# Kernel optimization log

Measured on AMD Instinct MI355X. Metric: run time of the kernel, lower is better.

Reference implementation:

```python
import jax, jax.numpy as jnp
import numpy as np

B, T, C = 4, 2048, 1024
H = 16
HD = C // H  # 64


def setup_inputs() -> dict:
    key = jax.random.key(0)
    ks = jax.random.split(key, 5)
    s = 0.02
    return {
        "x": jax.random.normal(ks[0], (B, T, C), jnp.float32),
        "qkv_w": jax.random.normal(ks[1], (3 * C, C), jnp.float32) * s,
        "qkv_b": jax.random.normal(ks[2], (3 * C,), jnp.float32) * s,
        "out_w": jax.random.normal(ks[3], (C, C), jnp.float32) * s,
        "out_b": jax.random.normal(ks[4], (C,), jnp.float32) * s,
    }


def reference(x, qkv_w, qkv_b, out_w, out_b):
    b, t, c = x.shape
    # qkv projection (torch Linear: x @ W^T + b)
    qkv = x @ qkv_w.T + qkv_b                      # (b, t, 3c)
    q, k, v = jnp.split(qkv, 3, axis=-1)
    def rsh(a):
        return a.reshape(b, t, H, HD).transpose(0, 2, 1, 3)  # (b, h, t, hd)
    q, k, v = rsh(q), rsh(k), rsh(v)
    scale = 1.0 / jnp.sqrt(jnp.float32(HD))
    attn = jnp.einsum('bhqd,bhkd->bhqk', q, k) * scale       # (b, h, t, t)
    causal = jnp.tril(jnp.ones((t, t), dtype=bool))
    attn = jnp.where(causal[None, None], attn, -jnp.inf)
    attn = jax.nn.softmax(attn, axis=-1)
    out = jnp.einsum('bhqk,bhkd->bhqd', attn, v)             # (b, h, t, hd)
    out = out.transpose(0, 2, 1, 3).reshape(b, t, c)
    return out @ out_w.T + out_b
```

## Files before the change

### kernel.cpp

```cpp
#include <hip/hip_runtime.h>

typedef __bf16 bf16x8 __attribute__((ext_vector_type(8)));
typedef __bf16 bf16x4 __attribute__((ext_vector_type(4)));
typedef float f32x4 __attribute__((ext_vector_type(4)));

typedef const __attribute__((address_space(1))) void* gptr_t;
typedef __attribute__((address_space(3))) void* lptr_t;

__device__ __forceinline__ f32x4 mfma16(bf16x8 a, bf16x8 b, f32x4 c) {
  return __builtin_amdgcn_mfma_f32_16x16x32_bf16(a, b, c, 0, 0, 0);
}

__device__ __forceinline__ void load_lds16(const __bf16* g, __bf16* l) {
  __builtin_amdgcn_global_load_lds((gptr_t)g, (lptr_t)l, 16, 0, 0);
}

__device__ __forceinline__ float fast_exp2(float x) {
#if __has_builtin(__builtin_amdgcn_exp2f)
  return __builtin_amdgcn_exp2f(x);
#else
  return exp2f(x);
#endif
}

__device__ __forceinline__ unsigned pack_bf16(float f0, float f1) {
  unsigned u0 = __builtin_bit_cast(unsigned, f0) + 0x8000u;
  unsigned u1 = __builtin_bit_cast(unsigned, f1) + 0x8000u;
  return __builtin_amdgcn_perm(u1, u0, 0x07060302);
}

__global__ __launch_bounds__(256) void convert3(
    const float* __restrict__ x, const float* __restrict__ w1,
    const float* __restrict__ w2, __bf16* __restrict__ xb,
    __bf16* __restrict__ w1b, __bf16* __restrict__ w2b) {
  int bid = blockIdx.x;
  const float* src;
  __bf16* dst;
  int base;
  if (bid < 4096) {
    src = x; dst = xb; base = bid;
  } else if (bid < 5632) {
    src = w1; dst = w1b; base = bid - 4096;
  } else {
    src = w2; dst = w2b; base = bid - 5632;
  }
  size_t off = (size_t)base * 2048 + threadIdx.x * 8;
  float4 v0 = *(const float4*)(src + off);
  float4 v1 = *(const float4*)(src + off + 4);
  bf16x8 o = {(__bf16)v0.x, (__bf16)v0.y, (__bf16)v0.z, (__bf16)v0.w,
              (__bf16)v1.x, (__bf16)v1.y, (__bf16)v1.z, (__bf16)v1.w};
  *(bf16x8*)(dst + off) = o;
}

template <bool C_BF16>
__global__ __launch_bounds__(256) void gemm_bt(
    const __bf16* __restrict__ A, const __bf16* __restrict__ B,
    const float* __restrict__ bias, void* __restrict__ Cv, int M, int N,
    int K, int qcols) {
  __shared__ __bf16 As[2][128 * 32];
  __shared__ __bf16 Bs[2][128 * 32];

  const int tid = threadIdx.x;
  const int wid = tid >> 6;
  const int lane = tid & 63;
  const int l15 = lane & 15;
  const int quad = lane >> 4;
  const int bm = blockIdx.y * 128;
  const int bn = blockIdx.x * 128;
  const int wm = (wid & 1) * 64;
  const int wn = (wid >> 1) * 64;

  const int srow = wid * 16 + (lane >> 2);
  const int schunk = (lane & 3) * 8;
  const __bf16* gA = A + (size_t)(bm + srow) * K + schunk;
  const __bf16* gB = B + (size_t)(bn + srow) * K + schunk;
  const int ldsoff = wid * 16 * 32;

  f32x4 acc[4][4] = {};

  load_lds16(gA, &As[0][ldsoff]);
  load_lds16(gA + (size_t)64 * K, &As[0][64 * 32 + ldsoff]);
  load_lds16(gB, &Bs[0][ldsoff]);
  load_lds16(gB + (size_t)64 * K, &Bs[0][64 * 32 + ldsoff]);

  const int niter = K >> 5;
  for (int it = 0; it < niter; ++it) {
    const int cur = it & 1;
    __syncthreads();
    if (it + 1 < niter) {
      int k0 = (it + 1) << 5;
      load_lds16(gA + k0, &As[1 - cur][ldsoff]);
      load_lds16(gA + k0 + (size_t)64 * K, &As[1 - cur][64 * 32 + ldsoff]);
      load_lds16(gB + k0, &Bs[1 - cur][ldsoff]);
      load_lds16(gB + k0 + (size_t)64 * K, &Bs[1 - cur][64 * 32 + ldsoff]);
    }
    bf16x8 af[4], bf[4];
#pragma unroll
    for (int i = 0; i < 4; ++i)
      af[i] = *(const bf16x8*)(&As[cur][(wm + i * 16 + l15) * 32 + quad * 8]);
#pragma unroll
    for (int i = 0; i < 4; ++i)
      bf[i] = *(const bf16x8*)(&Bs[cur][(wn + i * 16 + l15) * 32 + quad * 8]);
#pragma unroll
    for (int mt = 0; mt < 4; ++mt)
#pragma unroll
      for (int nt = 0; nt < 4; ++nt)
        acc[mt][nt] = mfma16(af[mt], bf[nt], acc[mt][nt]);
  }

  const float sc = (bn < qcols) ? 0.18033688011112043f : 1.0f;
#pragma unroll
  for (int mt = 0; mt < 4; ++mt) {
#pragma unroll
    for (int nt = 0; nt < 4; ++nt) {
      int gc = bn + wn + nt * 16 + l15;
      float bv = bias[gc];
#pragma unroll
      for (int r = 0; r < 4; ++r) {
        int gr = bm + wm + mt * 16 + quad * 4 + r;
        float val = (acc[mt][nt][r] + bv) * sc;
        if constexpr (C_BF16)
          ((__bf16*)Cv)[(size_t)gr * N + gc] = (__bf16)val;
        else
          ((float*)Cv)[(size_t)gr * N + gc] = val;
      }
    }
  }
}

template <bool MASK>
__device__ __forceinline__ void softmax_block(f32x4 (&s)[2][4],
                                              float (&lsum)[2][4],
                                              __bf16* __restrict__ psw,
                                              int kv0, int qrow_base, int quad,
                                              int l15) {
#pragma unroll
  for (int mt = 0; mt < 2; ++mt) {
#pragma unroll
    for (int r = 0; r < 4; ++r) {
      int prow = mt * 16 + quad * 4 + r;
      float p[4];
#pragma unroll
      for (int nt = 0; nt < 4; ++nt) {
        p[nt] = fast_exp2(s[mt][nt][r]);
        if constexpr (MASK) {
          if ((kv0 + nt * 16 + l15) > (qrow_base + prow)) p[nt] = 0.f;
        }
      }
      lsum[mt][r] += (p[0] + p[1]) + (p[2] + p[3]);
      uint2 w = {pack_bf16(p[0], p[1]), pack_bf16(p[2], p[3])};
      int o = ((l15 >> 1) ^ (prow & 7)) & 7;
      *(uint2*)(psw + prow * 64 + o * 8 + 4 * (l15 & 1)) = w;
    }
  }
}

__global__ __launch_bounds__(256) void attn_kernel(
    const __bf16* __restrict__ qkv, __bf16* __restrict__ out) {
  constexpr int T = 2048, C3 = 3072;
  constexpr int KVSTEP = 64 * C3;
  __shared__ __bf16 Ks[2][64 * 64];
  __shared__ __bf16 Vt[2][64 * 64];
  __shared__ __bf16 Ps[4][32 * 64];

  const int tid = threadIdx.x;
  const int wid = tid >> 6;
  const int lane = tid & 63;
  const int l15 = lane & 15;
  const int quad = lane >> 4;
  const int bh = blockIdx.x;
  const int pb = blockIdx.y;
  const int b = bh >> 4, h = bh & 15;
  const size_t rowbase = (size_t)b * T;

  const int kr = tid >> 3;
  const int kc = tid & 7;
  const int vj = tid >> 4;
  const int vn = tid & 15;

  const __bf16* gk_base = qkv + rowbase * C3 + 1024 + h * 64 + kr * C3 + kc * 8;
  const __bf16* gv_base = qkv + rowbase * C3 + 2048 + h * 64 + vj * C3 + vn * 4;

#pragma unroll 1
  for (int phase = 0; phase < 2; ++phase) {
    const int qp = phase == 0 ? pb : 15 - pb;
    const int q0 = qp * 128;
    const int ntiles = 2 * qp + 2;
    const int qrow_base = q0 + wid * 32;

    bf16x8 qf[2][2];
#pragma unroll
    for (int mt = 0; mt < 2; ++mt)
#pragma unroll
      for (int ksi = 0; ksi < 2; ++ksi)
        qf[mt][ksi] = *(const bf16x8*)(
            qkv + (rowbase + qrow_base + mt * 16 + l15) * C3 + h * 64 +
            ksi * 32 + quad * 8);

    f32x4 acc[2][4] = {};
    float lsum[2][4] = {};

    const __bf16* gk = gk_base;
    const __bf16* gv = gv_base;

    bf16x8 kreg[2];
    bf16x4 vreg[4];
    kreg[0] = *(const bf16x8*)(gk);
    kreg[1] = *(const bf16x8*)(gk + 32 * C3);
#pragma unroll
    for (int i = 0; i < 4; ++i)
      vreg[i] = *(const bf16x4*)(gv + i * 16 * C3);

    __syncthreads();

    for (int j = 0; j < ntiles; ++j) {
      __bf16* ksb = Ks[j & 1];
      __bf16* vtb = Vt[j & 1];
#pragma unroll
      for (int p = 0; p < 2; ++p) {
        int r = p * 32 + kr;
        *(bf16x8*)(ksb + r * 64 + ((kc ^ (r & 7)) * 8)) = kreg[p];
      }
#pragma unroll
      for (int dd = 0; dd < 4; ++dd) {
        int d = 4 * vn + dd;
        bf16x4 t = {vreg[0][dd], vreg[1][dd], vreg[2][dd], vreg[3][dd]};
        int o = ((vj >> 1) ^ (d & 7) ^ (d >> 3)) & 7;
        *(bf16x4*)(vtb + d * 64 + o * 8 + 4 * (vj & 1)) = t;
      }
      if (j + 1 < ntiles) {
        gk += KVSTEP;
        gv += KVSTEP;
        kreg[0] = *(const bf16x8*)(gk);
        kreg[1] = *(const bf16x8*)(gk + 32 * C3);
#pragma unroll
        for (int i = 0; i < 4; ++i)
          vreg[i] = *(const bf16x4*)(gv + i * 16 * C3);
      }
      __syncthreads();

      const int kv0 = j * 64;
      f32x4 s[2][4] = {};
#pragma unroll
      for (int nt = 0; nt < 4; ++nt) {
        int krow = nt * 16 + l15;
#pragma unroll
        for (int ksi = 0; ksi < 2; ++ksi) {
          bf16x8 kf = *(const bf16x8*)(
              ksb + krow * 64 + (((4 * ksi + quad) ^ (l15 & 7)) * 8));
#pragma unroll
          for (int mt = 0; mt < 2; ++mt)
            s[mt][nt] = mfma16(qf[mt][ksi], kf, s[mt][nt]);
        }
      }
      if ((kv0 + 63) > qrow_base)
        softmax_block<true>(s, lsum, Ps[wid], kv0, qrow_base, quad, l15);
      else
        softmax_block<false>(s, lsum, Ps[wid], kv0, qrow_base, quad, l15);

#pragma unroll
      for (int ksi = 0; ksi < 2; ++ksi) {
        bf16x8 pf[2];
#pragma unroll
        for (int mt = 0; mt < 2; ++mt) {
          int prow = mt * 16 + l15;
          pf[mt] = *(const bf16x8*)(
              Ps[wid] + prow * 64 + (((4 * ksi + quad) ^ (l15 & 7)) * 8));
        }
#pragma unroll
        for (int ntv = 0; ntv < 4; ++ntv) {
          int d = ntv * 16 + l15;
          int o = ((4 * ksi + quad) ^ (d & 7) ^ (d >> 3)) & 7;
          bf16x8 vf = *(const bf16x8*)(vtb + d * 64 + o * 8);
#pragma unroll
          for (int mt = 0; mt < 2; ++mt)
            acc[mt][ntv] = mfma16(pf[mt], vf, acc[mt][ntv]);
        }
      }
    }

#pragma unroll
    for (int mt = 0; mt < 2; ++mt)
#pragma unroll
      for (int r = 0; r < 4; ++r) {
        float l = lsum[mt][r];
        l += __shfl_xor(l, 1);
        l += __shfl_xor(l, 2);
        l += __shfl_xor(l, 4);
        l += __shfl_xor(l, 8);
        float inv = 1.0f / l;
        int row = qrow_base + mt * 16 + quad * 4 + r;
        size_t ob = (rowbase + row) * 1024 + h * 64;
#pragma unroll
        for (int ntv = 0; ntv < 4; ++ntv)
          out[ob + ntv * 16 + l15] = (__bf16)(acc[mt][ntv][r] * inv);
      }
  }
}

extern "C" void kernel_launch(void* const* d_in, const int* in_sizes, int n_in,
                              void* d_out, int out_size, void* d_ws,
                              size_t ws_size, hipStream_t stream) {
  const float* x = (const float*)d_in[0];
  const float* qkv_w = (const float*)d_in[1];
  const float* qkv_b = (const float*)d_in[2];
  const float* out_w = (const float*)d_in[3];
  const float* out_b = (const float*)d_in[4];
  float* out = (float*)d_out;

  __bf16* qkv_ws = (__bf16*)d_ws;
  __bf16* attn_ws = qkv_ws + (size_t)8192 * 3072;
  __bf16* xb = attn_ws + (size_t)8192 * 1024;
  __bf16* wqb = xb + (size_t)8192 * 1024;
  __bf16* wob = wqb + (size_t)3072 * 1024;

  convert3<<<6144, 256, 0, stream>>>(x, qkv_w, out_w, xb, wqb, wob);
  gemm_bt<true><<<dim3(24, 64), 256, 0, stream>>>(xb, wqb, qkv_b, qkv_ws,
                                                  8192, 3072, 1024, 1024);
  attn_kernel<<<dim3(64, 8), 256, 0, stream>>>(qkv_ws, attn_ws);
  gemm_bt<false><<<dim3(8, 64), 256, 0, stream>>>(attn_ws, wob, out_b, out,
                                                  8192, 1024, 1024, 0);
}
```

Baseline: 246.0 us.

## Swizzle GEMM LDS tiles and hoist attention LDS offset computation

The GEMM kernel now applies an XOR swizzle to the 16-byte chunk position, both when global_load_lds writes A/B tiles into LDS and when fragments are read back. This is meant to cut LDS bank conflicts on the fragment reads. The attention kernel precomputes all swizzled LDS store and load offsets once before the phase loop, so the inner tile loop no longer recomputes the index arithmetic. The cost is extra registers held across the loop, which may affect occupancy.

```diff
diff --git a/kernel.cpp b/kernel.cpp
--- a/kernel.cpp
+++ b/kernel.cpp
@@ -71,10 +71,12 @@
   const int wn = (wid >> 1) * 64;
 
   const int srow = wid * 16 + (lane >> 2);
-  const int schunk = (lane & 3) * 8;
+  const int schunk = ((lane & 3) ^ ((lane >> 3) & 3)) * 8;
   const __bf16* gA = A + (size_t)(bm + srow) * K + schunk;
   const __bf16* gB = B + (size_t)(bn + srow) * K + schunk;
   const int ldsoff = wid * 16 * 32;
+
+  const int fsl = (quad ^ ((l15 >> 1) & 3)) * 8;
 
   f32x4 acc[4][4] = {};
 
@@ -97,10 +99,10 @@
     bf16x8 af[4], bf[4];
 #pragma unroll
     for (int i = 0; i < 4; ++i)
-      af[i] = *(const bf16x8*)(&As[cur][(wm + i * 16 + l15) * 32 + quad * 8]);
+      af[i] = *(const bf16x8*)(&As[cur][(wm + i * 16 + l15) * 32 + fsl]);
 #pragma unroll
     for (int i = 0; i < 4; ++i)
-      bf[i] = *(const bf16x8*)(&Bs[cur][(wn + i * 16 + l15) * 32 + quad * 8]);
+      bf[i] = *(const bf16x8*)(&Bs[cur][(wn + i * 16 + l15) * 32 + fsl]);
 #pragma unroll
     for (int mt = 0; mt < 4; ++mt)
 #pragma unroll
@@ -181,6 +183,39 @@
   const __bf16* gk_base = qkv + rowbase * C3 + 1024 + h * 64 + kr * C3 + kc * 8;
   const __bf16* gv_base = qkv + rowbase * C3 + 2048 + h * 64 + vj * C3 + vn * 4;
 
+  int ks_st0 = kr * 64 + ((kc ^ (kr & 7)) * 8);
+  int ks_st1 = (kr + 32) * 64 + ((kc ^ ((kr + 32) & 7)) * 8);
+  int vt_st[4];
+#pragma unroll
+  for (int dd = 0; dd < 4; ++dd) {
+    int d = 4 * vn + dd;
+    vt_st[dd] = d * 64 + ((((vj >> 1) ^ (d & 7) ^ (d >> 3)) & 7) * 8) +
+                4 * (vj & 1);
+  }
+  int kf_off[4][2];
+#pragma unroll
+  for (int nt = 0; nt < 4; ++nt)
+#pragma unroll
+    for (int ksi = 0; ksi < 2; ++ksi)
+      kf_off[nt][ksi] =
+          (nt * 16 + l15) * 64 + (((4 * ksi + quad) ^ (l15 & 7)) * 8);
+  int pf_off[2][2];
+#pragma unroll
+  for (int mt = 0; mt < 2; ++mt)
+#pragma unroll
+    for (int ksi = 0; ksi < 2; ++ksi)
+      pf_off[mt][ksi] =
+          (mt * 16 + l15) * 64 + (((4 * ksi + quad) ^ (l15 & 7)) * 8);
+  int vf_off[4][2];
+#pragma unroll
+  for (int ntv = 0; ntv < 4; ++ntv)
+#pragma unroll
+    for (int ksi = 0; ksi < 2; ++ksi) {
+      int d = ntv * 16 + l15;
+      vf_off[ntv][ksi] =
+          d * 64 + ((((4 * ksi + quad) ^ (d & 7) ^ (d >> 3)) & 7) * 8);
+    }
+
 #pragma unroll 1
   for (int phase = 0; phase < 2; ++phase) {
     const int qp = phase == 0 ? pb : 15 - pb;
@@ -216,17 +251,12 @@
     for (int j = 0; j < ntiles; ++j) {
       __bf16* ksb = Ks[j & 1];
       __bf16* vtb = Vt[j & 1];
-#pragma unroll
-      for (int p = 0; p < 2; ++p) {
-        int r = p * 32 + kr;
-        *(bf16x8*)(ksb + r * 64 + ((kc ^ (r & 7)) * 8)) = kreg[p];
-      }
+      *(bf16x8*)(ksb + ks_st0) = kreg[0];
+      *(bf16x8*)(ksb + ks_st1) = kreg[1];
 #pragma unroll
       for (int dd = 0; dd < 4; ++dd) {
-        int d = 4 * vn + dd;
         bf16x4 t = {vreg[0][dd], vreg[1][dd], vreg[2][dd], vreg[3][dd]};
-        int o = ((vj >> 1) ^ (d & 7) ^ (d >> 3)) & 7;
-        *(bf16x4*)(vtb + d * 64 + o * 8 + 4 * (vj & 1)) = t;
+        *(bf16x4*)(vtb + vt_st[dd]) = t;
       }
       if (j + 1 < ntiles) {
         gk += KVSTEP;
@@ -243,11 +273,9 @@
       f32x4 s[2][4] = {};
 #pragma unroll
       for (int nt = 0; nt < 4; ++nt) {
-        int krow = nt * 16 + l15;
 #pragma unroll
         for (int ksi = 0; ksi < 2; ++ksi) {
-          bf16x8 kf = *(const bf16x8*)(
-              ksb + krow * 64 + (((4 * ksi + quad) ^ (l15 & 7)) * 8));
+          bf16x8 kf = *(const bf16x8*)(ksb + kf_off[nt][ksi]);
 #pragma unroll
           for (int mt = 0; mt < 2; ++mt)
             s[mt][nt] = mfma16(qf[mt][ksi], kf, s[mt][nt]);
@@ -262,16 +290,11 @@
       for (int ksi = 0; ksi < 2; ++ksi) {
         bf16x8 pf[2];
 #pragma unroll
-        for (int mt = 0; mt < 2; ++mt) {
-          int prow = mt * 16 + l15;
-          pf[mt] = *(const bf16x8*)(
-              Ps[wid] + prow * 64 + (((4 * ksi + quad) ^ (l15 & 7)) * 8));
-        }
+        for (int mt = 0; mt < 2; ++mt)
+          pf[mt] = *(const bf16x8*)(Ps[wid] + pf_off[mt][ksi]);
 #pragma unroll
         for (int ntv = 0; ntv < 4; ++ntv) {
-          int d = ntv * 16 + l15;
-          int o = ((4 * ksi + quad) ^ (d & 7) ^ (d >> 3)) & 7;
-          bf16x8 vf = *(const bf16x8*)(vtb + d * 64 + o * 8);
+          bf16x8 vf = *(const bf16x8*)(vtb + vf_off[ntv][ksi]);
 #pragma unroll
           for (int mt = 0; mt < 2; ++mt)
             acc[mt][ntv] = mfma16(pf[mt], vf, acc[mt][ntv]);
```

New measurement: 243.3 us. Within noise of the previous version (-1.1%).
